# Performance work log

Hardware: AMD Instinct MI355X
Metric: run time of the kernel (lower is better)

## Reference

```python
import jax, jax.numpy as jnp
import numpy as np

# Dims: N nodes, F input feats, H1/H2 gcn widths, M modules (= n_class)
N, F, H1, H2, M = 150000, 500, 200, 8, 8


def sign01(p):
    # MySign.forward: (p > 0).float()
    return (p > 0).astype(p.dtype)


def setup_inputs() -> dict:
    key = jax.random.key(0)
    ks = jax.random.split(key, 11)
    s = 0.05  # weight scale for numerical sanity
    return {
        "x":     jax.random.normal(ks[0], (N, F), jnp.float32),
        # frozen shared GCN body
        "W1":    jax.random.normal(ks[1], (F, H1), jnp.float32) * s,
        "b1":    jnp.zeros((H1,), jnp.float32),
        "W2":    jax.random.normal(ks[2], (H1, H2), jnp.float32) * s,
        "b2":    jnp.zeros((H2,), jnp.float32),
        # per-module sign masks (torch.randn init)
        "mask1": jax.random.normal(ks[3], (M, H1), jnp.float32),
        "mask2": jax.random.normal(ks[4], (M, H2), jnp.float32),
        # per-module heads: Linear(8,8) -> ReLU -> Linear(8,1)
        "hw1":   jax.random.normal(ks[5], (M, H2, 8), jnp.float32) * s,
        "hb1":   jnp.zeros((M, 8), jnp.float32),
        "hw2":   jax.random.normal(ks[6], (M, 8), jnp.float32) * s,
        "hb2":   jnp.zeros((M,), jnp.float32),
    }


def reference(x, W1, b1, W2, b2, mask1, mask2, hw1, hb1, hw2, hb2):
    # Shared gcn1 is identical across modules -> compute once ([N,H1])
    h1 = jax.nn.relu(x @ W1 + b1)
    m1 = sign01(mask1)              # [M,H1]
    m2 = sign01(mask2)              # [M,H2]
    # per-module: mask1 * h1, then shared gcn2, then mask2 ([M,N,H2])
    h2 = jnp.einsum('nk,mk,kc->mnc', h1, m1, W2) + b2
    z = h2 * m2[:, None, :]
    # tiny 2-layer head per module, sigmoid output ([M,N])
    hid = jax.nn.relu(jnp.einsum('mnc,mch->mnh', z, hw1) + hb1[:, None, :])
    out = jax.nn.sigmoid(jnp.einsum('mnh,mh->mn', hid, hw2) + hb2[:, None])
    return out.T                    # [N, M] == torch.cat(preds, dim=1)
```

## Files before the change

kernel.cpp:

```cpp
#include <hip/hip_runtime.h>
#include <stdint.h>

#define N_NODES 150000
#define F_IN    500
#define H1      200
#define C1      224
#define J2      64
#define K2      224
#define BM      128
#define NTHREADS 512

#define WS0_ELEMS 114688
#define WS1_ELEMS 14336

typedef short short8 __attribute__((ext_vector_type(8)));
typedef float float4v __attribute__((ext_vector_type(4)));

__device__ __forceinline__ short f2bf(float f) {
    uint32_t u = __float_as_uint(f);
    u = (u + 0x7FFFu + ((u >> 16) & 1u)) >> 16;
    return (short)u;
}
__device__ __forceinline__ float bf2f(short s) {
    return __uint_as_float(((uint32_t)(uint16_t)s) << 16);
}

__global__ __launch_bounds__(256) void prep_kernel(
    const float* __restrict__ W1, const float* __restrict__ W2,
    const float* __restrict__ mask1, short* __restrict__ ws)
{
    int idx = blockIdx.x * 256 + threadIdx.x;
    if (idx < WS0_ELEMS) {
        int ks = idx / 7168;
        int r  = idx - ks * 7168;
        int c  = r >> 5;
        int k  = ks * 32 + (r & 31);
        float v = (c < H1 && k < F_IN) ? W1[k * H1 + c] : 0.f;
        ws[idx] = f2bf(v);
    } else if (idx < WS0_ELEMS + WS1_ELEMS) {
        int r = idx - WS0_ELEMS;
        int j = r / K2;
        int k = r - j * K2;
        int m = j >> 3, c = j & 7;
        float v = 0.f;
        if (k < H1 && mask1[m * H1 + k] > 0.f) v = W2[k * 8 + c];
        ws[idx] = f2bf(v);
    }
}

__global__ __launch_bounds__(NTHREADS, 4) void fused_kernel(
    const float* __restrict__ x,  const float* __restrict__ b1,
    const float* __restrict__ b2, const float* __restrict__ mask2,
    const float* __restrict__ hw1, const float* __restrict__ hb1,
    const float* __restrict__ hw2, const float* __restrict__ hb2,
    const short* __restrict__ ws, float* __restrict__ out)
{
    __shared__ __align__(16) char lds[81920];
    short* as  = (short*)lds;
    short* bt  = (short*)(lds + 8192);
    short* zs  = (short*)lds;
    float* smalls = (float*)(lds + 18432);
    short* h1s = (short*)(lds + 22528);

    const int tid  = threadIdx.x;
    const int lane = tid & 63;
    const int wid  = tid >> 6;
    const int l15  = lane & 15;
    const int l4   = lane >> 4;
    const int n0   = blockIdx.x * BM;

    const int wrow = wid >> 1;
    const int wcol = wid & 1;

    float4v acc[2][7];
    #pragma unroll
    for (int i = 0; i < 2; ++i)
        #pragma unroll
        for (int j = 0; j < 7; ++j) acc[i][j] = (float4v)0.f;

    const int srow = tid >> 2;
    const int su   = tid & 3;
    const long grow = (long)(n0 + srow) * F_IN;
    const bool rowok = (n0 + srow) < N_NODES;
    short* aswr = as + srow * 32 + ((su ^ ((srow >> 1) & 3)) * 8);

    const short* afrag[2];
    #pragma unroll
    for (int i = 0; i < 2; ++i) {
        int row = wrow * 32 + i * 16 + l15;
        afrag[i] = as + row * 32 + ((l4 ^ ((row >> 1) & 3)) * 8);
    }
    const short* bfrag[7];
    #pragma unroll
    for (int j = 0; j < 7; ++j) {
        int col = (wcol * 7 + j) * 16 + l15;
        bfrag[j] = bt + col * 32 + ((l4 ^ ((col >> 1) & 3)) * 8);
    }

    for (int ks = 0; ks < 16; ++ks) {
        __syncthreads();
        {
            int k0 = ks * 32 + su * 8;
            float xv[8];
            if (rowok && (k0 + 7) < F_IN) {
                const float4* p = (const float4*)(x + grow + k0);
                float4 a = p[0], b = p[1];
                xv[0]=a.x; xv[1]=a.y; xv[2]=a.z; xv[3]=a.w;
                xv[4]=b.x; xv[5]=b.y; xv[6]=b.z; xv[7]=b.w;
            } else {
                #pragma unroll
                for (int e = 0; e < 8; ++e)
                    xv[e] = (rowok && (k0 + e) < F_IN) ? x[grow + k0 + e] : 0.f;
            }
            short8 sv;
            #pragma unroll
            for (int e = 0; e < 8; ++e) sv[e] = f2bf(xv[e]);
            *(short8*)aswr = sv;
        }
        {
            const short* src = ws + ks * 7168;
            int uu = tid;
            {
                int c = uu >> 2, u = uu & 3;
                short8 w = *(const short8*)(src + uu * 8);
                *(short8*)(bt + c * 32 + ((u ^ ((c >> 1) & 3)) * 8)) = w;
            }
            uu = tid + NTHREADS;
            if (uu < 896) {
                int c = uu >> 2, u = uu & 3;
                short8 w = *(const short8*)(src + uu * 8);
                *(short8*)(bt + c * 32 + ((u ^ ((c >> 1) & 3)) * 8)) = w;
            }
        }
        __syncthreads();
        short8 a0 = *(const short8*)afrag[0];
        short8 a1 = *(const short8*)afrag[1];
        #pragma unroll
        for (int j = 0; j < 7; ++j) {
            short8 b = *(const short8*)bfrag[j];
            acc[0][j] = __builtin_amdgcn_mfma_f32_16x16x32_bf16(a0, b, acc[0][j], 0, 0, 0);
            acc[1][j] = __builtin_amdgcn_mfma_f32_16x16x32_bf16(a1, b, acc[1][j], 0, 0, 0);
        }
    }
    __syncthreads();

    for (int i = tid; i < 944; i += NTHREADS) {
        float v;
        if      (i < 224) v = (i < H1) ? b1[i] : 0.f;
        else if (i < 232) v = b2[i - 224];
        else if (i < 296) v = (mask2[i - 232] > 0.f) ? 1.f : 0.f;
        else if (i < 808) v = hw1[i - 296];
        else if (i < 872) v = hb1[i - 808];
        else if (i < 936) v = hw2[i - 872];
        else              v = hb2[i - 936];
        smalls[i] = v;
    }
    __syncthreads();

    #pragma unroll
    for (int j = 0; j < 7; ++j) {
        int col = (wcol * 7 + j) * 16 + l15;
        float bb = smalls[col];
        #pragma unroll
        for (int i = 0; i < 2; ++i) {
            int rowb = wrow * 32 + i * 16 + l4 * 4;
            #pragma unroll
            for (int r = 0; r < 4; ++r) {
                float v = acc[i][j][r] + bb;
                v = v > 0.f ? v : 0.f;
                h1s[(rowb + r) * 232 + col] = f2bf(v);
            }
        }
    }

    short8 b2f[7][2];
    #pragma unroll
    for (int s = 0; s < 7; ++s)
        #pragma unroll
        for (int jj = 0; jj < 2; ++jj) {
            int j = (wcol * 2 + jj) * 16 + l15;
            b2f[s][jj] = *(const short8*)(ws + WS0_ELEMS + j * K2 + s * 32 + l4 * 8);
        }
    __syncthreads();

    float4v acc2[2][2];
    #pragma unroll
    for (int i = 0; i < 2; ++i)
        #pragma unroll
        for (int jj = 0; jj < 2; ++jj) acc2[i][jj] = (float4v)0.f;

    #pragma unroll
    for (int s = 0; s < 7; ++s) {
        short8 a2[2];
        #pragma unroll
        for (int i = 0; i < 2; ++i) {
            int row = wrow * 32 + i * 16 + l15;
            a2[i] = *(const short8*)(h1s + row * 232 + s * 32 + l4 * 8);
        }
        #pragma unroll
        for (int i = 0; i < 2; ++i)
            #pragma unroll
            for (int jj = 0; jj < 2; ++jj)
                acc2[i][jj] = __builtin_amdgcn_mfma_f32_16x16x32_bf16(a2[i], b2f[s][jj], acc2[i][jj], 0, 0, 0);
    }

    #pragma unroll
    for (int jj = 0; jj < 2; ++jj) {
        int j = (wcol * 2 + jj) * 16 + l15;
        int c = j & 7;
        float bias  = smalls[224 + c];
        float scale = smalls[232 + j];
        #pragma unroll
        for (int i = 0; i < 2; ++i) {
            int rowb = wrow * 32 + i * 16 + l4 * 4;
            #pragma unroll
            for (int r = 0; r < 4; ++r) {
                float z = (acc2[i][jj][r] + bias) * scale;
                zs[(rowb + r) * 72 + j] = f2bf(z);
            }
        }
    }
    __syncthreads();

    {
        int n  = tid >> 2;
        int m0 = (tid & 3) * 2;
        short8 za = *(const short8*)(zs + n * 72 + m0 * 8);
        short8 zb = *(const short8*)(zs + n * 72 + m0 * 8 + 8);
        float o[2];
        #pragma unroll
        for (int mm = 0; mm < 2; ++mm) {
            int m = m0 + mm;
            float zv[8];
            #pragma unroll
            for (int c = 0; c < 8; ++c) zv[c] = bf2f(mm == 0 ? za[c] : zb[c]);
            float hid[8];
            #pragma unroll
            for (int h = 0; h < 8; ++h) hid[h] = smalls[808 + m * 8 + h];
            #pragma unroll
            for (int c = 0; c < 8; ++c) {
                float zc = zv[c];
                const float* w = smalls + 296 + (m * 8 + c) * 8;
                #pragma unroll
                for (int h = 0; h < 8; ++h) hid[h] += zc * w[h];
            }
            float u = smalls[936 + m];
            #pragma unroll
            for (int h = 0; h < 8; ++h) {
                float hv = hid[h] > 0.f ? hid[h] : 0.f;
                u += hv * smalls[872 + m * 8 + h];
            }
            o[mm] = 1.f / (1.f + __expf(-u));
        }
        int gn = n0 + n;
        if (gn < N_NODES) {
            float2 ov = make_float2(o[0], o[1]);
            *(float2*)(out + (long)gn * 8 + m0) = ov;
        }
    }
}

extern "C" void kernel_launch(void* const* d_in, const int* in_sizes, int n_in,
                              void* d_out, int out_size, void* d_ws, size_t ws_size,
                              hipStream_t stream)
{
    const float* x     = (const float*)d_in[0];
    const float* W1    = (const float*)d_in[1];
    const float* b1    = (const float*)d_in[2];
    const float* W2    = (const float*)d_in[3];
    const float* b2    = (const float*)d_in[4];
    const float* mask1 = (const float*)d_in[5];
    const float* mask2 = (const float*)d_in[6];
    const float* hw1   = (const float*)d_in[7];
    const float* hb1   = (const float*)d_in[8];
    const float* hw2   = (const float*)d_in[9];
    const float* hb2   = (const float*)d_in[10];
    short* ws  = (short*)d_ws;
    float* out = (float*)d_out;

    if (ws_size < (size_t)(WS0_ELEMS + WS1_ELEMS) * sizeof(short)) return;

    int prep_blocks = (WS0_ELEMS + WS1_ELEMS + 255) / 256;
    prep_kernel<<<prep_blocks, 256, 0, stream>>>(W1, W2, mask1, ws);

    int main_blocks = (N_NODES + BM - 1) / BM;
    fused_kernel<<<main_blocks, NTHREADS, 0, stream>>>(
        x, b1, b2, mask2, hw1, hb1, hw2, hb2, ws, out);
}
```

Before: 469.4 us.

## Double-buffer x and W1 tiles via async global-to-LDS loads

The main GEMM loop now uses global_load_lds to stream raw fp32 x tiles and pre-swizzled bf16 W1 tiles straight into double-buffered LDS. The next k-step is prefetched while MFMAs run on the current one, with vmcnt waits and barriers for ordering. The fp32-to-bf16 conversion moves from the global load path to the LDS fragment read. The W1 workspace is padded to 256 columns with an XOR swizzle built in the prep kernel, and h1 staging gets a new swizzle. The aim is to hide global load latency behind compute. In exchange, LDS use grows to 128KB per block, which cuts blocks per CU, and reads past column 500 of each x row rely on zero W1 rows to cancel.

Result: no change. 460.4 us (-1.9%).

```diff
diff --git a/kernel.cpp b/kernel.cpp
--- a/kernel.cpp
+++ b/kernel.cpp
@@ -1,17 +1,19 @@
 #include <hip/hip_runtime.h>
 #include <stdint.h>
 
-#define N_NODES 150000
-#define F_IN    500
-#define H1      200
-#define C1      224
-#define J2      64
-#define K2      224
-#define BM      128
+#define NN       150000
+#define FF       500
+#define XLIM     (NN*FF - 4)
 #define NTHREADS 512
-
-#define WS0_ELEMS 114688
+#define NSTEPS   16
+
+#define WS0_ELEMS 131072
 #define WS1_ELEMS 14336
+
+#define A_STEP   16384
+#define B_BASE   32768
+#define H1S_BASE 65536
+#define ZS_BASE  4096
 
 typedef short short8 __attribute__((ext_vector_type(8)));
 typedef float float4v __attribute__((ext_vector_type(4)));
@@ -31,46 +33,74 @@
 {
     int idx = blockIdx.x * 256 + threadIdx.x;
     if (idx < WS0_ELEMS) {
-        int ks = idx / 7168;
-        int r  = idx - ks * 7168;
+        int t  = idx >> 13;
+        int r  = idx & 8191;
         int c  = r >> 5;
-        int k  = ks * 32 + (r & 31);
-        float v = (c < H1 && k < F_IN) ? W1[k * H1 + c] : 0.f;
+        int e  = r & 31;
+        int p  = e >> 3, ee = e & 7;
+        int k  = t * 32 + ((p ^ (c & 3)) << 3) + ee;
+        float v = (c < 200 && k < 500) ? W1[k * 200 + c] : 0.f;
         ws[idx] = f2bf(v);
     } else if (idx < WS0_ELEMS + WS1_ELEMS) {
         int r = idx - WS0_ELEMS;
-        int j = r / K2;
-        int k = r - j * K2;
+        int j = r / 224;
+        int k = r - j * 224;
         int m = j >> 3, c = j & 7;
         float v = 0.f;
-        if (k < H1 && mask1[m * H1 + k] > 0.f) v = W2[k * 8 + c];
+        if (k < 200 && mask1[m * 200 + k] > 0.f) v = W2[k * 8 + c];
         ws[idx] = f2bf(v);
     }
 }
 
-__global__ __launch_bounds__(NTHREADS, 4) void fused_kernel(
+#define GL16(gp, loff) __builtin_amdgcn_global_load_lds(                         \
+    (const __attribute__((address_space(1))) uint32_t*)(gp),                     \
+    (__attribute__((address_space(3))) uint32_t*)(lds + (loff)), 16, 0, 0)
+
+__global__ __launch_bounds__(NTHREADS, 2) void fused_kernel(
     const float* __restrict__ x,  const float* __restrict__ b1,
     const float* __restrict__ b2, const float* __restrict__ mask2,
     const float* __restrict__ hw1, const float* __restrict__ hb1,
     const float* __restrict__ hw2, const float* __restrict__ hb2,
     const short* __restrict__ ws, float* __restrict__ out)
 {
-    __shared__ __align__(16) char lds[81920];
-    short* as  = (short*)lds;
-    short* bt  = (short*)(lds + 8192);
-    short* zs  = (short*)lds;
-    float* smalls = (float*)(lds + 18432);
-    short* h1s = (short*)(lds + 22528);
-
+    __shared__ __align__(16) char lds[131072];
     const int tid  = threadIdx.x;
     const int lane = tid & 63;
-    const int wid  = tid >> 6;
+    const int w    = tid >> 6;
     const int l15  = lane & 15;
     const int l4   = lane >> 4;
-    const int n0   = blockIdx.x * BM;
-
-    const int wrow = wid >> 1;
-    const int wcol = wid & 1;
+    const int n0   = blockIdx.x * 128;
+    const int wrow = w >> 1;
+    const int wcol = w & 1;
+
+    int baseA[2];
+    #pragma unroll
+    for (int q = 0; q < 2; ++q) {
+        int r  = w * 16 + q * 8 + (lane >> 3);
+        int p  = lane & 7;
+        int rg = n0 + r; if (rg > NN - 1) rg = NN - 1;
+        baseA[q] = rg * FF + ((p ^ (r & 7)) << 2);
+    }
+    const int dst0 = w * 2048;
+    const int dst1 = w * 2048 + 1024;
+    const short* srcB0 = ws + w * 1024 + lane * 8;
+    const short* srcB1 = srcB0 + 512;
+
+    int offA[2][2], offB[7];
+    #pragma unroll
+    for (int i = 0; i < 2; ++i) {
+        int r = wrow * 32 + i * 16 + l15;
+        #pragma unroll
+        for (int j = 0; j < 2; ++j) {
+            int u = 2 * l4 + j;
+            offA[i][j] = r * 128 + ((u ^ (r & 7)) << 4);
+        }
+    }
+    #pragma unroll
+    for (int j = 0; j < 7; ++j) {
+        int c = wcol * 112 + j * 16 + l15;
+        offB[j] = c * 64 + ((l4 ^ (c & 3)) << 4);
+    }
 
     float4v acc[2][7];
     #pragma unroll
@@ -78,75 +108,58 @@
         #pragma unroll
         for (int j = 0; j < 7; ++j) acc[i][j] = (float4v)0.f;
 
-    const int srow = tid >> 2;
-    const int su   = tid & 3;
-    const long grow = (long)(n0 + srow) * F_IN;
-    const bool rowok = (n0 + srow) < N_NODES;
-    short* aswr = as + srow * 32 + ((su ^ ((srow >> 1) & 3)) * 8);
-
-    const short* afrag[2];
-    #pragma unroll
-    for (int i = 0; i < 2; ++i) {
-        int row = wrow * 32 + i * 16 + l15;
-        afrag[i] = as + row * 32 + ((l4 ^ ((row >> 1) & 3)) * 8);
-    }
-    const short* bfrag[7];
-    #pragma unroll
-    for (int j = 0; j < 7; ++j) {
-        int col = (wcol * 7 + j) * 16 + l15;
-        bfrag[j] = bt + col * 32 + ((l4 ^ ((col >> 1) & 3)) * 8);
-    }
-
-    for (int ks = 0; ks < 16; ++ks) {
-        __syncthreads();
-        {
-            int k0 = ks * 32 + su * 8;
-            float xv[8];
-            if (rowok && (k0 + 7) < F_IN) {
-                const float4* p = (const float4*)(x + grow + k0);
-                float4 a = p[0], b = p[1];
-                xv[0]=a.x; xv[1]=a.y; xv[2]=a.z; xv[3]=a.w;
-                xv[4]=b.x; xv[5]=b.y; xv[6]=b.z; xv[7]=b.w;
-            } else {
-                #pragma unroll
-                for (int e = 0; e < 8; ++e)
-                    xv[e] = (rowok && (k0 + e) < F_IN) ? x[grow + k0 + e] : 0.f;
-            }
-            short8 sv;
-            #pragma unroll
-            for (int e = 0; e < 8; ++e) sv[e] = f2bf(xv[e]);
-            *(short8*)aswr = sv;
-        }
-        {
-            const short* src = ws + ks * 7168;
-            int uu = tid;
-            {
-                int c = uu >> 2, u = uu & 3;
-                short8 w = *(const short8*)(src + uu * 8);
-                *(short8*)(bt + c * 32 + ((u ^ ((c >> 1) & 3)) * 8)) = w;
-            }
-            uu = tid + NTHREADS;
-            if (uu < 896) {
-                int c = uu >> 2, u = uu & 3;
-                short8 w = *(const short8*)(src + uu * 8);
-                *(short8*)(bt + c * 32 + ((u ^ ((c >> 1) & 3)) * 8)) = w;
-            }
-        }
-        __syncthreads();
-        short8 a0 = *(const short8*)afrag[0];
-        short8 a1 = *(const short8*)afrag[1];
+    {
+        int i0 = baseA[0]; if (i0 > XLIM) i0 = XLIM;
+        int i1 = baseA[1]; if (i1 > XLIM) i1 = XLIM;
+        GL16(x + i0, dst0);
+        GL16(x + i1, dst1);
+        GL16(srcB0, B_BASE + dst0);
+        GL16(srcB1, B_BASE + dst1);
+    }
+    #pragma unroll
+    for (int t = 0; t < NSTEPS; ++t) {
+        const int sel = t & 1;
+        if (t < NSTEPS - 1) {
+            const int o = (sel ^ 1) * A_STEP;
+            int i0 = baseA[0] + (t + 1) * 32; if (i0 > XLIM) i0 = XLIM;
+            int i1 = baseA[1] + (t + 1) * 32; if (i1 > XLIM) i1 = XLIM;
+            GL16(x + i0, o + dst0);
+            GL16(x + i1, o + dst1);
+            GL16(srcB0 + (t + 1) * 8192, B_BASE + o + dst0);
+            GL16(srcB1 + (t + 1) * 8192, B_BASE + o + dst1);
+            asm volatile("s_waitcnt vmcnt(4)" ::: "memory");
+        } else {
+            asm volatile("s_waitcnt vmcnt(0)" ::: "memory");
+        }
+        __builtin_amdgcn_s_barrier();
+        asm volatile("" ::: "memory");
+
+        const char* pa = lds + sel * A_STEP;
+        const char* pb = lds + B_BASE + sel * A_STEP;
+        float4v a00 = *(const float4v*)(pa + offA[0][0]);
+        float4v a01 = *(const float4v*)(pa + offA[0][1]);
+        float4v a10 = *(const float4v*)(pa + offA[1][0]);
+        float4v a11 = *(const float4v*)(pa + offA[1][1]);
+        short8 a0, a1;
+        #pragma unroll
+        for (int e = 0; e < 4; ++e) { a0[e] = f2bf(a00[e]); a0[4+e] = f2bf(a01[e]); }
+        #pragma unroll
+        for (int e = 0; e < 4; ++e) { a1[e] = f2bf(a10[e]); a1[4+e] = f2bf(a11[e]); }
         #pragma unroll
         for (int j = 0; j < 7; ++j) {
-            short8 b = *(const short8*)bfrag[j];
+            short8 b = *(const short8*)(pb + offB[j]);
             acc[0][j] = __builtin_amdgcn_mfma_f32_16x16x32_bf16(a0, b, acc[0][j], 0, 0, 0);
             acc[1][j] = __builtin_amdgcn_mfma_f32_16x16x32_bf16(a1, b, acc[1][j], 0, 0, 0);
         }
-    }
-    __syncthreads();
-
+        asm volatile("" ::: "memory");
+        __builtin_amdgcn_s_barrier();
+        asm volatile("" ::: "memory");
+    }
+
+    float* smalls = (float*)lds;
     for (int i = tid; i < 944; i += NTHREADS) {
         float v;
-        if      (i < 224) v = (i < H1) ? b1[i] : 0.f;
+        if      (i < 224) v = (i < 200) ? b1[i] : 0.f;
         else if (i < 232) v = b2[i - 224];
         else if (i < 296) v = (mask2[i - 232] > 0.f) ? 1.f : 0.f;
         else if (i < 808) v = hw1[i - 296];
@@ -161,14 +174,16 @@
     for (int j = 0; j < 7; ++j) {
         int col = (wcol * 7 + j) * 16 + l15;
         float bb = smalls[col];
+        int u = col >> 3, lo = (col & 7) * 2;
         #pragma unroll
         for (int i = 0; i < 2; ++i) {
             int rowb = wrow * 32 + i * 16 + l4 * 4;
             #pragma unroll
             for (int r = 0; r < 4; ++r) {
+                int row = rowb + r;
                 float v = acc[i][j][r] + bb;
                 v = v > 0.f ? v : 0.f;
-                h1s[(rowb + r) * 232 + col] = f2bf(v);
+                *(short*)(lds + H1S_BASE + row * 512 + ((u ^ (row & 7)) << 4) + lo) = f2bf(v);
             }
         }
     }
@@ -179,7 +194,7 @@
         #pragma unroll
         for (int jj = 0; jj < 2; ++jj) {
             int j = (wcol * 2 + jj) * 16 + l15;
-            b2f[s][jj] = *(const short8*)(ws + WS0_ELEMS + j * K2 + s * 32 + l4 * 8);
+            b2f[s][jj] = *(const short8*)(ws + WS0_ELEMS + j * 224 + s * 32 + l4 * 8);
         }
     __syncthreads();
 
@@ -195,7 +210,8 @@
         #pragma unroll
         for (int i = 0; i < 2; ++i) {
             int row = wrow * 32 + i * 16 + l15;
-            a2[i] = *(const short8*)(h1s + row * 232 + s * 32 + l4 * 8);
+            int u = s * 4 + l4;
+            a2[i] = *(const short8*)(lds + H1S_BASE + row * 512 + ((u ^ (row & 7)) << 4));
         }
         #pragma unroll
         for (int i = 0; i < 2; ++i)
@@ -204,6 +220,7 @@
                 acc2[i][jj] = __builtin_amdgcn_mfma_f32_16x16x32_bf16(a2[i], b2f[s][jj], acc2[i][jj], 0, 0, 0);
     }
 
+    short* zs = (short*)(lds + ZS_BASE);
     #pragma unroll
     for (int jj = 0; jj < 2; ++jj) {
         int j = (wcol * 2 + jj) * 16 + l15;
@@ -231,18 +248,15 @@
         #pragma unroll
         for (int mm = 0; mm < 2; ++mm) {
             int m = m0 + mm;
-            float zv[8];
-            #pragma unroll
-            for (int c = 0; c < 8; ++c) zv[c] = bf2f(mm == 0 ? za[c] : zb[c]);
             float hid[8];
             #pragma unroll
             for (int h = 0; h < 8; ++h) hid[h] = smalls[808 + m * 8 + h];
             #pragma unroll
             for (int c = 0; c < 8; ++c) {
-                float zc = zv[c];
-                const float* w = smalls + 296 + (m * 8 + c) * 8;
+                float zc = bf2f(mm == 0 ? za[c] : zb[c]);
+                const float* wv = smalls + 296 + (m * 8 + c) * 8;
                 #pragma unroll
-                for (int h = 0; h < 8; ++h) hid[h] += zc * w[h];
+                for (int h = 0; h < 8; ++h) hid[h] += zc * wv[h];
             }
             float u = smalls[936 + m];
             #pragma unroll
@@ -253,7 +267,7 @@
             o[mm] = 1.f / (1.f + __expf(-u));
         }
         int gn = n0 + n;
-        if (gn < N_NODES) {
+        if (gn < NN) {
             float2 ov = make_float2(o[0], o[1]);
             *(float2*)(out + (long)gn * 8 + m0) = ov;
         }
@@ -283,7 +297,7 @@
     int prep_blocks = (WS0_ELEMS + WS1_ELEMS + 255) / 256;
     prep_kernel<<<prep_blocks, 256, 0, stream>>>(W1, W2, mask1, ws);
 
-    int main_blocks = (N_NODES + BM - 1) / BM;
+    int main_blocks = (NN + 127) / 128;
     fused_kernel<<<main_blocks, NTHREADS, 0, stream>>>(
         x, b1, b2, mask2, hw1, hb1, hw2, hb2, ws, out);
 }
```
